# Kernel tuning notes

Hardware: AMD Instinct MI355X
Metric: run time of the kernel (lower is better)

The kernel has to match this reference:

```python
import jax, jax.numpy as jnp
import numpy as np

B, NQ, NK, H = 4, 2048, 2048, 512
TEMP = 1.0


def setup_inputs() -> dict:
    key = jax.random.key(0)
    ks = jax.random.split(key, 13)
    s = 0.02
    inp = {
        "query_feat": jax.random.normal(ks[0], (B, NQ, H), jnp.float32),
        "key_feat": jax.random.normal(ks[1], (B, NK, H), jnp.float32),
        "qm_uncert": jax.random.normal(ks[2], (B, NQ), jnp.float32),
        "md_uncert": jax.random.normal(ks[3], (B, NK), jnp.float32),
        "Wq": jax.random.normal(ks[4], (H, H), jnp.float32) * s,
        "bq": jnp.zeros((H,), jnp.float32),
        "Wk": jax.random.normal(ks[5], (H, H), jnp.float32) * s,
        "bk": jnp.zeros((H,), jnp.float32),
        "Wv": jax.random.normal(ks[6], (H, H), jnp.float32) * s,
        "bv": jnp.zeros((H,), jnp.float32),
        "Wo": jax.random.normal(ks[7], (H, H), jnp.float32) * s,
        "bo": jnp.zeros((H,), jnp.float32),
        "tau": jnp.float32(1.0),
    }
    return inp


def reference(query_feat, key_feat, qm_uncert, md_uncert,
              Wq, bq, Wk, bk, Wv, bv, Wo, bo, tau):
    h = query_feat.shape[-1]
    Q = query_feat @ Wq.T + bq          # [B,Nq,H]
    K = key_feat @ Wk.T + bk            # [B,Nk,H]
    V = key_feat @ Wv.T + bv            # [B,Nk,H]

    # scaled dot-product logits
    logits = jnp.einsum('bqh,bkh->bqk', Q, K) / jnp.sqrt(jnp.asarray(h, logits_dtype(Q)))

    # uncertainty weight: sigmoid(tau * (qm_i + md_j)), then sanitize (mult mode)
    u = jax.nn.sigmoid(tau * (qm_uncert[:, :, None] + md_uncert[:, None, :]))
    u = jnp.nan_to_num(u, nan=1.0, posinf=1e6, neginf=1e-6)
    u = jnp.clip(u, 1e-6, 1e6)
    row_sum = jnp.sum(jnp.abs(u), axis=-1, keepdims=True)
    u = jnp.where(row_sum <= 1e-12, jnp.asarray(1e-6, u.dtype), u)

    logits = (logits * u) / TEMP

    # rows fully masked to -1e9 get zeroed (no mask here, but kept for faithfulness)
    all_masked = jnp.all(logits == -1e9, axis=-1, keepdims=True)
    logits = jnp.where(all_masked, jnp.zeros_like(logits), logits)

    attn = jax.nn.softmax(logits, axis=-1)  # dropout p=0 -> identity
    att = jnp.einsum('bqk,bkh->bqh', attn, V)
    out = att @ Wo.T + bo
    return out, attn


def logits_dtype(x):
    return x.dtype
```

## Files before the change

kernel.cpp:

```cpp
#include <hip/hip_runtime.h>
#include <stdint.h>

#define DEVI static __device__ __forceinline__

typedef unsigned short u16;
typedef short bf16x8 __attribute__((ext_vector_type(8)));
typedef u16 u16x8 __attribute__((ext_vector_type(8)));
typedef u16 u16x4 __attribute__((ext_vector_type(4)));
typedef float f32x4 __attribute__((ext_vector_type(4)));

DEVI u16 f2bf(float f) {
    uint32_t u = __builtin_bit_cast(uint32_t, f);
    u += 0x7FFFu + ((u >> 16) & 1u);
    return (u16)(u >> 16);
}
DEVI float bf2f(u16 u) { return __builtin_bit_cast(float, (uint32_t)u << 16); }

DEVI void xcd_remap(int& bx, int& by, int& bz, bool yfast) {
    int nx = gridDim.x, ny = gridDim.y, nz = gridDim.z;
    int nwg = nx * ny * nz;
    if (nwg & 7) return;
    int f = yfast ? (by + ny * (bx + nx * bz))
                  : (bx + nx * (by + ny * bz));
    int fp = (f >> 3) + (nwg >> 3) * (f & 7);
    if (yfast) { by = fp % ny; bx = (fp / ny) % nx; bz = fp / (ny * nx); }
    else       { bx = fp % nx; by = (fp / nx) % ny; bz = fp / (nx * ny); }
}

struct GemmArgs {
    const void* A;
    const void* A2;
    long long aStrideBytes;
    int lda;
    const u16* Bm;
    long long bStrideElts;
    int ldb;
    int K;
    const float* bias; const float* bias2; const float* bias3;
    u16* outB;
    float* outF;
    long long outFStride;
    const float* qm; const float* md; const float* tauPtr; float scale;
    float* partials;
    const float* invsPtr;
    float* invsOut;
    u16* vt;
};

enum { EPI_PROJ3 = 0, EPI_LOGITS = 1, EPI_LOGITSB = 2, EPI_PV = 3, EPI_OUT = 4 };

template <int EPI, int AMODE, int TM, bool U2>
__global__ __launch_bounds__(256, 4) void gemm_bt(GemmArgs p) {
    constexpr int NB = U2 ? 2 : 1;
    constexpr int NF = (TM == 128) ? 4 : 2;
    __shared__ u16 As[NB][TM * 32];
    __shared__ u16 Bs[NB][128 * 32];
    __shared__ float redBuf[2][128];
    __shared__ float sInvLds[128];

    const int tid = threadIdx.x;
    const int lane = tid & 63;
    const int wave = tid >> 6;
    const int g = lane >> 4, lr = lane & 15;
    const int waveRowBase = (TM == 128) ? (wave >> 1) * 64 : 0;
    const int waveColBase = (TM == 128) ? (wave & 1) * 64 : wave * 32;

    int bxR = blockIdx.x, byR = blockIdx.y, bzR = blockIdx.z;
    xcd_remap(bxR, byR, bzR, EPI == EPI_OUT);
    const int z = bzR;
    const int rowBase = bxR * TM;
    const int colBase = byR * 128;

    int batch = z, koff = 0;
    if constexpr (EPI == EPI_PV) { batch = z & 3; koff = (z >> 2) * p.K; }

    const char* Abase;
    const float* bias = p.bias;
    const u16* Bbase;
    if constexpr (EPI == EPI_PROJ3) {
        Abase = (const char*)(z == 0 ? p.A : p.A2);
        Bbase = p.Bm + (size_t)z * 512 * 512;
        bias = (z == 0) ? p.bias : (z == 1 ? p.bias2 : p.bias3);
    } else {
        Abase = (const char*)p.A + (size_t)batch * p.aStrideBytes + (size_t)koff * (AMODE == 1 ? 4 : 2);
        Bbase = p.Bm + (size_t)batch * p.bStrideElts + koff;
    }

    if constexpr (EPI == EPI_PV && AMODE == 0) {
        if (byR == 4) {
            if (tid < 128) {
                const float* pp = p.partials + ((size_t)batch * 2048 + rowBase + tid) * 16;
                float s = 0.f;
                #pragma unroll
                for (int t = 0; t < 16; ++t) s += pp[t];
                float inv = 1.0f / s;
                sInvLds[tid] = inv;
                p.invsOut[batch * 2048 + rowBase + tid] = inv;
            }
            __syncthreads();
            const u16* e = (const u16*)Abase + (size_t)rowBase * 2048;
            float* attnOut = p.outF + (size_t)batch * p.outFStride + (size_t)rowBase * 2048 + koff;
            #pragma unroll 4
            for (int it = 0; it < 64; ++it) {
                int cc = it * 256 + tid;
                int row = cc >> 7, colc = (cc & 127) * 8;
                float s = sInvLds[row];
                u16x8 v = *(const u16x8*)(e + (size_t)row * 2048 + colc);
                f32x4 f0, f1;
                f0[0] = bf2f(v[0]) * s; f0[1] = bf2f(v[1]) * s;
                f0[2] = bf2f(v[2]) * s; f0[3] = bf2f(v[3]) * s;
                f1[0] = bf2f(v[4]) * s; f1[1] = bf2f(v[5]) * s;
                f1[2] = bf2f(v[6]) * s; f1[3] = bf2f(v[7]) * s;
                float* dst = attnOut + (size_t)row * 2048 + colc;
                __builtin_nontemporal_store(f0, (f32x4*)dst);
                __builtin_nontemporal_store(f1, (f32x4*)dst + 1);
            }
            return;
        }
    }

    f32x4 acc[4][NF] = {};

    const int arow2 = tid >> 2, kh2 = (tid & 3) << 3;
    const u16* pa0 = nullptr; const u16* pa1 = nullptr; float sInv = 1.0f;
    if constexpr (AMODE == 2) {
        pa0 = (const u16*)p.A + (size_t)(rowBase + arow2) * 512 + kh2;
        pa1 = pa0 + (size_t)8192 * 512;
        sInv = p.invsPtr ? p.invsPtr[rowBase + arow2] : 1.0f;
    }

    const int nk = p.K >> 5;
    for (int kt = 0; kt < nk; kt += NB) {
        const int kb = kt << 5;
        float4 areg[4]; u16x8 a0, a1;
        if constexpr (AMODE == 1) {
            const float* Af = (const float*)Abase;
            const int arow = tid >> 1, kh = (tid & 1) << 4;
            const float* src = Af + (size_t)(rowBase + arow) * p.lda + kb + kh;
            #pragma unroll
            for (int j = 0; j < 4; ++j) areg[j] = ((const float4*)src)[j];
        } else if constexpr (AMODE == 2) {
            a0 = *(const u16x8*)(pa0 + kb);
            a1 = *(const u16x8*)(pa1 + kb);
        }
        __syncthreads();
        if constexpr (AMODE == 1) {
            const int arow = tid >> 1, kh = (tid & 1) << 4;
            u16 tmp[16];
            #pragma unroll
            for (int j = 0; j < 4; ++j) {
                tmp[4 * j + 0] = f2bf(areg[j].x);
                tmp[4 * j + 1] = f2bf(areg[j].y);
                tmp[4 * j + 2] = f2bf(areg[j].z);
                tmp[4 * j + 3] = f2bf(areg[j].w);
            }
            #pragma unroll
            for (int h = 0; h < 2; ++h)
                *(u16x8*)&As[0][arow * 32 + kh + h * 8] = *(u16x8*)&tmp[h * 8];
        } else if constexpr (AMODE == 2) {
            u16 tmp[8];
            #pragma unroll
            for (int j = 0; j < 8; ++j)
                tmp[j] = f2bf((bf2f(a0[j]) + bf2f(a1[j])) * sInv);
            *(u16x8*)&As[0][arow2 * 32 + kh2] = *(u16x8*)tmp;
        } else {
            #pragma unroll
            for (int b = 0; b < NB; ++b)
                #pragma unroll
                for (int i = 0; i < TM / 64; ++i) {
                    int c = i * 256 + tid;
                    const u16* gp = (const u16*)Abase + (size_t)(rowBase + (c >> 2)) * p.lda + kb + b * 32 + (c & 3) * 8;
                    char* lp = (char*)&As[b][0] + (i * 256 + wave * 64) * 16;
                    __builtin_amdgcn_global_load_lds((const __attribute__((address_space(1))) void*)gp,
                                                     (__attribute__((address_space(3))) void*)lp, 16, 0, 0);
                }
        }
        #pragma unroll
        for (int b = 0; b < NB; ++b)
            #pragma unroll
            for (int i = 0; i < 2; ++i) {
                int c = i * 256 + tid;
                const u16* gp = Bbase + (size_t)(colBase + (c >> 2)) * p.ldb + kb + b * 32 + (c & 3) * 8;
                char* lp = (char*)&Bs[b][0] + (i * 256 + wave * 64) * 16;
                __builtin_amdgcn_global_load_lds((const __attribute__((address_space(1))) void*)gp,
                                                 (__attribute__((address_space(3))) void*)lp, 16, 0, 0);
            }
        __syncthreads();

        #pragma unroll
        for (int b = 0; b < NB; ++b) {
            bf16x8 af[4], bfr[NF];
            #pragma unroll
            for (int m = 0; m < 4; ++m)
                af[m] = *(const bf16x8*)&As[b][(waveRowBase + m * 16 + lr) * 32 + g * 8];
            #pragma unroll
            for (int n = 0; n < NF; ++n)
                bfr[n] = *(const bf16x8*)&Bs[b][(waveColBase + n * 16 + lr) * 32 + g * 8];
            #pragma unroll
            for (int m = 0; m < 4; ++m)
                #pragma unroll
                for (int n = 0; n < NF; ++n)
                    acc[m][n] = __builtin_amdgcn_mfma_f32_16x16x32_bf16(af[m], bfr[n], acc[m][n], 0, 0, 0);
        }
    }

    const int rB = rowBase + waveRowBase;
    const int cB = colBase + waveColBase;

    if constexpr (EPI == EPI_PROJ3) {
        if (z < 2) {
            u16* dst = p.outB + (size_t)z * 8192 * 512;
            #pragma unroll
            for (int n = 0; n < NF; ++n) {
                int col = cB + n * 16 + lr;
                float bv = bias[col];
                #pragma unroll
                for (int m = 0; m < 4; ++m) {
                    int r0 = rB + m * 16 + g * 4;
                    #pragma unroll
                    for (int i = 0; i < 4; ++i)
                        dst[(size_t)(r0 + i) * 512 + col] = f2bf(acc[m][n][i] + bv);
                }
            }
        } else {
            #pragma unroll
            for (int n = 0; n < NF; ++n) {
                int col = cB + n * 16 + lr;
                float bv = bias[col];
                #pragma unroll
                for (int m = 0; m < 4; ++m) {
                    int r0 = rB + m * 16 + g * 4;
                    int b = r0 >> 11, k0 = r0 & 2047;
                    u16x4 pk;
                    #pragma unroll
                    for (int i = 0; i < 4; ++i) pk[i] = f2bf(acc[m][n][i] + bv);
                    *(u16x4*)&p.vt[((size_t)b * 512 + col) * 2048 + k0] = pk;
                }
            }
        }
    } else if constexpr (EPI == EPI_LOGITS || EPI == EPI_LOGITSB) {
        const float* eqB = p.qm + z * 2048;
        const float* emB = p.md + z * 2048;
        float* outRow = p.outF + (size_t)z * p.outFStride;
        float emv[NF];
        #pragma unroll
        for (int n = 0; n < NF; ++n) emv[n] = emB[cB + n * 16 + lr];
        #pragma unroll
        for (int m = 0; m < 4; ++m) {
            int r0 = rB + m * 16 + g * 4;
            #pragma unroll
            for (int i = 0; i < 4; ++i) {
                int q = r0 + i;
                float eqv = eqB[q];
                float rs = 0.f;
                #pragma unroll
                for (int n = 0; n < NF; ++n) {
                    float u = 1.0f / (1.0f + eqv * emv[n]);
                    u = fmaxf(u, 1e-6f);
                    float e = __expf(acc[m][n][i] * p.scale * u);
                    if (EPI == EPI_LOGITSB)
                        p.outB[((size_t)(z * 2048 + q)) * 2048 + cB + n * 16 + lr] = f2bf(e);
                    else
                        outRow[(size_t)q * 2048 + cB + n * 16 + lr] = e;
                    rs += e;
                }
                #pragma unroll
                for (int off = 1; off < 16; off <<= 1) rs += __shfl_xor(rs, off, 64);
                if (lr == 0) redBuf[wave & 1][waveRowBase + m * 16 + g * 4 + i] = rs;
            }
        }
        __syncthreads();
        if (tid < 128) {
            float s = redBuf[0][tid] + redBuf[1][tid];
            int q = rowBase + tid;
            p.partials[((size_t)z * 2048 + q) * 16 + byR] = s;
        }
    } else if constexpr (EPI == EPI_PV) {
        const int split = z >> 2;
        u16* dst = p.outB + (size_t)split * 8192 * 512;
        #pragma unroll
        for (int n = 0; n < NF; ++n) {
            int col = cB + n * 16 + lr;
            #pragma unroll
            for (int m = 0; m < 4; ++m) {
                int r0 = rB + m * 16 + g * 4;
                size_t gr = (size_t)batch * 2048 + r0;
                #pragma unroll
                for (int i = 0; i < 4; ++i)
                    dst[(gr + i) * 512 + col] = f2bf(acc[m][n][i]);
            }
        }
    } else {
        #pragma unroll
        for (int n = 0; n < NF; ++n) {
            int col = cB + n * 16 + lr;
            float bv = p.bias[col];
            #pragma unroll
            for (int m = 0; m < 4; ++m) {
                int r0 = rB + m * 16 + g * 4;
                #pragma unroll
                for (int i = 0; i < 4; ++i)
                    __builtin_nontemporal_store(acc[m][n][i] + bv, &p.outF[(size_t)(r0 + i) * 512 + col]);
            }
        }
    }
}

__global__ void cvt_all3(const float* Wq, const float* Wk, const float* Wv, const float* Wo,
                         const float* qf, const float* kf,
                         const float* qm, const float* md, const float* tauPtr,
                         u16* wdst, u16* qdst, u16* kdst,
                         float* eq, float* em) {
    if (blockIdx.x >= gridDim.x - 64) {
        int j = (blockIdx.x - (gridDim.x - 64)) * 256 + threadIdx.x;
        float tau = *tauPtr;
        if (j < 8192) eq[j] = __expf(-tau * qm[j]);
        else          em[j - 8192] = __expf(-tau * md[j - 8192]);
        return;
    }
    const size_t WSZ = (size_t)512 * 512;
    const size_t FSZ = (size_t)8192 * 512;
    size_t i = ((size_t)blockIdx.x * 256 + threadIdx.x) * 4;
    const float* src; u16* dstp;
    if (i < 4 * WSZ) {
        int w = (int)(i / WSZ);
        src = (w == 0 ? Wq : w == 1 ? Wk : w == 2 ? Wv : Wo) + (i - (size_t)w * WSZ);
        dstp = wdst + i;
    } else if (i < 4 * WSZ + FSZ) {
        size_t off = i - 4 * WSZ;
        src = qf + off; dstp = qdst + off;
    } else {
        size_t off = i - 4 * WSZ - FSZ;
        src = kf + off; dstp = kdst + off;
    }
    float4 v = *(const float4*)src;
    u16x4 u = { f2bf(v.x), f2bf(v.y), f2bf(v.z), f2bf(v.w) };
    *(u16x4*)dstp = u;
}

__global__ void rowsum_inv(const float* __restrict__ partials, float* __restrict__ invs) {
    int r = blockIdx.x * 256 + threadIdx.x;
    float s = 0.f;
    #pragma unroll
    for (int t = 0; t < 16; ++t) s += partials[r * 16 + t];
    invs[r] = 1.0f / s;
}

__global__ void normalize_attn(float* __restrict__ attn, const float* __restrict__ invs) {
    size_t i4 = (size_t)blockIdx.x * 256 + threadIdx.x;
    int row = (int)(i4 >> 9);
    float s = invs[row];
    float4 v = ((const float4*)attn)[i4];
    v.x *= s; v.y *= s; v.z *= s; v.w *= s;
    ((float4*)attn)[i4] = v;
}

extern "C" void kernel_launch(void* const* d_in, const int* in_sizes, int n_in,
                              void* d_out, int out_size, void* d_ws, size_t ws_size,
                              hipStream_t stream) {
    const float* qf  = (const float*)d_in[0];
    const float* kf  = (const float*)d_in[1];
    const float* qm  = (const float*)d_in[2];
    const float* md  = (const float*)d_in[3];
    const float* Wq  = (const float*)d_in[4];
    const float* bq  = (const float*)d_in[5];
    const float* Wk  = (const float*)d_in[6];
    const float* bk  = (const float*)d_in[7];
    const float* Wv  = (const float*)d_in[8];
    const float* bv  = (const float*)d_in[9];
    const float* Wo  = (const float*)d_in[10];
    const float* bo  = (const float*)d_in[11];
    const float* tau = (const float*)d_in[12];

    float* out  = (float*)d_out;
    float* attn = out + (size_t)4 * 2048 * 512;

    const size_t NV = (size_t)8192 * 512;
    u16* Qb   = (u16*)d_ws;
    u16* Kb   = Qb + NV;
    u16* Vtb  = Kb + NV;
    u16* Wqb  = Vtb + NV;
    u16* Wob  = Wqb + (size_t)3 * 512 * 512;
    float* partials = (float*)(Wqb + (size_t)4 * 512 * 512);
    float* invs = partials + (size_t)8192 * 16;
    float* eq = invs + 8192;
    float* em = eq + 8192;
    u16* attE = (u16*)(em + 8192);
    u16* qfB  = attE + (size_t)4 * 2048 * 2048;
    u16* kfB  = qfB + NV;
    size_t need = (size_t)((char*)(kfB + NV) - (char*)d_ws);
    const bool big = ws_size >= need;

    u16* partialPV = Qb;

    dim3 blk(256);

    GemmArgs a = {};
    a.lda = 512; a.ldb = 512; a.K = 512;
    a.bias = bq; a.bias2 = bk; a.bias3 = bv;
    a.outB = Qb; a.vt = Vtb;
    if (big) {
        cvt_all3<<<dim3(9280), blk, 0, stream>>>(Wq, Wk, Wv, Wo, qf, kf, qm, md, tau,
                                                 Wqb, qfB, kfB, eq, em);
        a.A = qfB; a.A2 = kfB; a.Bm = Wqb;
        gemm_bt<EPI_PROJ3, 0, 128, true><<<dim3(64, 4, 3), blk, 0, stream>>>(a);
    } else {
        cvt_all3<<<dim3(1088), blk, 0, stream>>>(Wq, Wk, Wv, Wo, qf, kf, qm, md, tau,
                                                 Wqb, nullptr, nullptr, eq, em);
        a.A = qf; a.A2 = kf; a.Bm = Wqb;
        gemm_bt<EPI_PROJ3, 1, 128, false><<<dim3(64, 4, 3), blk, 0, stream>>>(a);
    }

    GemmArgs lg = {};
    lg.A = Qb; lg.aStrideBytes = (long long)2048 * 512 * 2; lg.lda = 512;
    lg.Bm = Kb; lg.bStrideElts = (long long)2048 * 512; lg.ldb = 512;
    lg.K = 512;
    lg.qm = eq; lg.md = em; lg.tauPtr = tau;
    lg.scale = 0.04419417382415922f;
    lg.partials = partials;
    if (big) {
        lg.outB = attE;
        gemm_bt<EPI_LOGITSB, 0, 128, true><<<dim3(16, 16, 4), blk, 0, stream>>>(lg);
    } else {
        lg.outF = attn; lg.outFStride = (long long)2048 * 2048;
        gemm_bt<EPI_LOGITS, 0, 128, true><<<dim3(16, 16, 4), blk, 0, stream>>>(lg);
    }

    GemmArgs pv = {};
    pv.Bm = Vtb; pv.bStrideElts = (long long)512 * 2048; pv.ldb = 2048;
    pv.K = 1024; pv.outB = partialPV; pv.lda = 2048;
    pv.partials = partials; pv.invsOut = invs;
    if (big) {
        pv.A = attE; pv.aStrideBytes = (long long)2048 * 2048 * 2;
        pv.outF = attn; pv.outFStride = (long long)2048 * 2048;
        gemm_bt<EPI_PV, 0, 128, true><<<dim3(16, 5, 8), blk, 0, stream>>>(pv);
    } else {
        rowsum_inv<<<dim3(32), blk, 0, stream>>>(partials, invs);
        normalize_attn<<<dim3(16384), blk, 0, stream>>>(attn, invs);
        pv.A = attn; pv.aStrideBytes = (long long)2048 * 2048 * 4;
        gemm_bt<EPI_PV, 1, 128, false><<<dim3(16, 4, 8), blk, 0, stream>>>(pv);
    }

    GemmArgs og = {};
    og.A = partialPV; og.lda = 512;
    og.Bm = Wob; og.ldb = 512;
    og.K = 512; og.bias = bo; og.outF = out;
    og.invsPtr = big ? invs : nullptr;
    gemm_bt<EPI_OUT, 2, 64, false><<<dim3(128, 4, 1), blk, 0, stream>>>(og);
}
```

Baseline: 123.3 us.

## Fuse attention normalization into PV epilogue and use exp2 with prescaled logits

The normalized attn write, previously done by a dedicated extra column of blocks in the PV grid, is now done in the epilogue of every PV block, each covering a 256-column slice. The row inverse sums are computed beforehand by a separate rowsum_inv launch on the big path. Logits are scaled by log2(e) so exp2f replaces __expf. This spreads the bandwidth-heavy attn write across all blocks instead of a few stragglers, at the cost of an extra small kernel launch and a longer PV epilogue.

```diff
diff --git a/kernel.cpp b/kernel.cpp
--- a/kernel.cpp
+++ b/kernel.cpp
@@ -56,7 +56,6 @@
     __shared__ u16 As[NB][TM * 32];
     __shared__ u16 Bs[NB][128 * 32];
     __shared__ float redBuf[2][128];
-    __shared__ float sInvLds[128];
 
     const int tid = threadIdx.x;
     const int lane = tid & 63;
@@ -84,39 +83,6 @@
     } else {
         Abase = (const char*)p.A + (size_t)batch * p.aStrideBytes + (size_t)koff * (AMODE == 1 ? 4 : 2);
         Bbase = p.Bm + (size_t)batch * p.bStrideElts + koff;
-    }
-
-    if constexpr (EPI == EPI_PV && AMODE == 0) {
-        if (byR == 4) {
-            if (tid < 128) {
-                const float* pp = p.partials + ((size_t)batch * 2048 + rowBase + tid) * 16;
-                float s = 0.f;
-                #pragma unroll
-                for (int t = 0; t < 16; ++t) s += pp[t];
-                float inv = 1.0f / s;
-                sInvLds[tid] = inv;
-                p.invsOut[batch * 2048 + rowBase + tid] = inv;
-            }
-            __syncthreads();
-            const u16* e = (const u16*)Abase + (size_t)rowBase * 2048;
-            float* attnOut = p.outF + (size_t)batch * p.outFStride + (size_t)rowBase * 2048 + koff;
-            #pragma unroll 4
-            for (int it = 0; it < 64; ++it) {
-                int cc = it * 256 + tid;
-                int row = cc >> 7, colc = (cc & 127) * 8;
-                float s = sInvLds[row];
-                u16x8 v = *(const u16x8*)(e + (size_t)row * 2048 + colc);
-                f32x4 f0, f1;
-                f0[0] = bf2f(v[0]) * s; f0[1] = bf2f(v[1]) * s;
-                f0[2] = bf2f(v[2]) * s; f0[3] = bf2f(v[3]) * s;
-                f1[0] = bf2f(v[4]) * s; f1[1] = bf2f(v[5]) * s;
-                f1[2] = bf2f(v[6]) * s; f1[3] = bf2f(v[7]) * s;
-                float* dst = attnOut + (size_t)row * 2048 + colc;
-                __builtin_nontemporal_store(f0, (f32x4*)dst);
-                __builtin_nontemporal_store(f1, (f32x4*)dst + 1);
-            }
-            return;
-        }
     }
 
     f32x4 acc[4][NF] = {};
@@ -257,7 +223,7 @@
                 for (int n = 0; n < NF; ++n) {
                     float u = 1.0f / (1.0f + eqv * emv[n]);
                     u = fmaxf(u, 1e-6f);
-                    float e = __expf(acc[m][n][i] * p.scale * u);
+                    float e = exp2f(acc[m][n][i] * p.scale * u);
                     if (EPI == EPI_LOGITSB)
                         p.outB[((size_t)(z * 2048 + q)) * 2048 + cB + n * 16 + lr] = f2bf(e);
                     else
@@ -288,6 +254,27 @@
                 #pragma unroll
                 for (int i = 0; i < 4; ++i)
                     dst[(gr + i) * 512 + col] = f2bf(acc[m][n][i]);
+            }
+        }
+        if constexpr (AMODE == 0) {
+            const int sl = byR * 2 + split;
+            const u16* eB = (const u16*)p.A + ((size_t)batch * 2048 + rowBase) * 2048 + sl * 256;
+            float* aOut = p.outF + (size_t)batch * p.outFStride + (size_t)rowBase * 2048 + sl * 256;
+            const float* invR = p.invsPtr + batch * 2048 + rowBase;
+            #pragma unroll 4
+            for (int it = 0; it < 16; ++it) {
+                int cc = it * 256 + tid;
+                int row = cc >> 5, colc = (cc & 31) * 8;
+                float s = invR[row];
+                u16x8 v = *(const u16x8*)(eB + (size_t)row * 2048 + colc);
+                f32x4 f0, f1;
+                f0[0] = bf2f(v[0]) * s; f0[1] = bf2f(v[1]) * s;
+                f0[2] = bf2f(v[2]) * s; f0[3] = bf2f(v[3]) * s;
+                f1[0] = bf2f(v[4]) * s; f1[1] = bf2f(v[5]) * s;
+                f1[2] = bf2f(v[6]) * s; f1[3] = bf2f(v[7]) * s;
+                float* dstF = aOut + (size_t)row * 2048 + colc;
+                __builtin_nontemporal_store(f0, (f32x4*)dstF);
+                __builtin_nontemporal_store(f1, (f32x4*)dstF + 1);
             }
         }
     } else {
@@ -416,7 +403,7 @@
     lg.Bm = Kb; lg.bStrideElts = (long long)2048 * 512; lg.ldb = 512;
     lg.K = 512;
     lg.qm = eq; lg.md = em; lg.tauPtr = tau;
-    lg.scale = 0.04419417382415922f;
+    lg.scale = 0.04419417382415922f * 1.4426950408889634f;
     lg.partials = partials;
     if (big) {
         lg.outB = attE;
@@ -426,16 +413,17 @@
         gemm_bt<EPI_LOGITS, 0, 128, true><<<dim3(16, 16, 4), blk, 0, stream>>>(lg);
     }
 
+    rowsum_inv<<<dim3(32), blk, 0, stream>>>(partials, invs);
+
     GemmArgs pv = {};
     pv.Bm = Vtb; pv.bStrideElts = (long long)512 * 2048; pv.ldb = 2048;
     pv.K = 1024; pv.outB = partialPV; pv.lda = 2048;
-    pv.partials = partials; pv.invsOut = invs;
+    pv.invsPtr = invs;
     if (big) {
         pv.A = attE; pv.aStrideBytes = (long long)2048 * 2048 * 2;
         pv.outF = attn; pv.outFStride = (long long)2048 * 2048;
-        gemm_bt<EPI_PV, 0, 128, true><<<dim3(16, 5, 8), blk, 0, stream>>>(pv);
-    } else {
-        rowsum_inv<<<dim3(32), blk, 0, stream>>>(partials, invs);
+        gemm_bt<EPI_PV, 0, 128, true><<<dim3(16, 4, 8), blk, 0, stream>>>(pv);
+    } else {
         normalize_attn<<<dim3(16384), blk, 0, stream>>>(attn, invs);
         pv.A = attn; pv.aStrideBytes = (long long)2048 * 2048 * 4;
         gemm_bt<EPI_PV, 1, 128, false><<<dim3(16, 4, 8), blk, 0, stream>>>(pv);
```

Result: slower. 136.6 us (+10.8%).
